# Performance work log

Hardware: AMD Instinct MI355X
Metric: run time of the kernel (lower is better)

Reference implementation:

```python
import jax, jax.numpy as jnp
import numpy as np

B, C_IN, N, F_OUT = 16, 128, 2048, 64
NEG_SLOPE = 0.33
MASK_VAL = -9e15


def setup_inputs() -> dict:
    key = jax.random.key(0)
    k1, k2, k3, k4 = jax.random.split(key, 4)
    h = jax.random.normal(k1, (B, C_IN, N, 1), dtype=jnp.float32)
    g = jax.random.normal(k2, (B, 1, N, N), dtype=jnp.float32)
    # xavier_uniform with gain=1.414
    gain = 1.414
    lim_W = gain * np.sqrt(6.0 / (C_IN + F_OUT))
    W = jax.random.uniform(k3, (C_IN, F_OUT), minval=-lim_W, maxval=lim_W, dtype=jnp.float32)
    lim_a = gain * np.sqrt(6.0 / (2 * F_OUT + 1))
    a = jax.random.uniform(k4, (2 * F_OUT, 1), minval=-lim_a, maxval=lim_a, dtype=jnp.float32)
    return {"h": h, "g": g, "W": W, "a": a}


def reference(h, g, W, a):
    # h: [B, C, N, 1] -> node features [B, N, C]
    hn = jnp.transpose(h[..., 0], (0, 2, 1))
    Wh = jnp.einsum('bnc,cf->bnf', hn, W)  # [B, N, F]
    F = W.shape[1]
    a1, a2 = a[:F, 0], a[F:, 0]
    # additive attention: e[i,j] = leakyrelu(Wh[i]@a1 + Wh[j]@a2)
    e = jax.nn.leaky_relu((Wh @ a1)[:, :, None] + (Wh @ a2)[:, None, :], NEG_SLOPE)  # [B,N,N]
    mask = g[:, 0] > 0  # [B, N, N]
    attn = jax.nn.softmax(jnp.where(mask, e, MASK_VAL), axis=-1)
    h_prime = jnp.einsum('bij,bjf->bif', attn, Wh)  # [B, N, F]
    return jnp.transpose(h_prime, (0, 2, 1))[..., None]  # [B, F, N, 1]
```

## Files before the change

### kernel.cpp

```cpp
#include <hip/hip_runtime.h>
#include <hip/hip_bf16.h>

#define NB 16
#define NC 128
#define NN 2048
#define NF 64
#define NEG_SLOPE 0.33f
#define EXP_K 1.4426950408889634f

typedef float    f32x2 __attribute__((ext_vector_type(2)));
typedef float    f32x4 __attribute__((ext_vector_type(4)));
typedef _Float16 f16x4 __attribute__((ext_vector_type(4)));
typedef _Float16 f16x8 __attribute__((ext_vector_type(8)));

__device__ __forceinline__ float lrelu(float x) {
    return fmaxf(x, x * NEG_SLOPE);
}
__device__ __forceinline__ float rdfl(float v) {
    return __int_as_float(__builtin_amdgcn_readfirstlane(__float_as_int(v)));
}

__global__ __launch_bounds__(256) void k_precompute(
    const float* __restrict__ h, const float* __restrict__ W,
    const float* __restrict__ a, _Float16* __restrict__ wht,
    float* __restrict__ s1g, float* __restrict__ s2g)
{
    __shared__ float Wl[64 * 64];
    __shared__ float ht[64 * 129];

    const int t = threadIdx.x;
    const int b = blockIdx.x >> 5;
    const int n0 = (blockIdx.x & 31) << 6;
    const int lane = t & 63, cg = t >> 6;

    #pragma unroll 8
    for (int k = 0; k < 32; ++k) {
        const int c = cg * 32 + k;
        ht[lane * 129 + c] = h[(size_t)(b * NC + c) * NN + n0 + lane];
    }

    const int fg = t & 15, ns = t >> 4;
    f32x4 acc[4] = {};
    for (int half = 0; half < 2; ++half) {
        if (half) __syncthreads();
        #pragma unroll
        for (int k = 0; k < 4; ++k) {
            const int idx = k * 1024 + t * 4;
            *(f32x4*)&Wl[idx] = *(const f32x4*)&W[half * 4096 + idx];
        }
        __syncthreads();
        #pragma unroll 4
        for (int c2 = 0; c2 < 64; ++c2) {
            const f32x4 wv = *(const f32x4*)&Wl[c2 * 64 + fg * 4];
            #pragma unroll
            for (int m = 0; m < 4; ++m) {
                const float hv = ht[(ns * 4 + m) * 129 + half * 64 + c2];
                acc[m] += wv * hv;
            }
        }
    }

    const f32x4 a1v = *(const f32x4*)&a[fg * 4];
    const f32x4 a2v = *(const f32x4*)&a[NF + fg * 4];
    #pragma unroll
    for (int m = 0; m < 4; ++m) {
        float p1 = acc[m].x * a1v.x + acc[m].y * a1v.y + acc[m].z * a1v.z + acc[m].w * a1v.w;
        float p2 = acc[m].x * a2v.x + acc[m].y * a2v.y + acc[m].z * a2v.z + acc[m].w * a2v.w;
        #pragma unroll
        for (int d = 1; d < 16; d <<= 1) {
            p1 += __shfl_xor(p1, d, 64);
            p2 += __shfl_xor(p2, d, 64);
        }
        if (fg == 0) {
            const int n = n0 + ns * 4 + m;
            s1g[(size_t)b * NN + n] = p1;
            s2g[(size_t)b * NN + n] = p2;
        }
    }
    #pragma unroll
    for (int q = 0; q < 4; ++q) {
        f16x4 v;
        v[0] = (_Float16)acc[0][q]; v[1] = (_Float16)acc[1][q];
        v[2] = (_Float16)acc[2][q]; v[3] = (_Float16)acc[3][q];
        const int f = fg * 4 + q;
        *(f16x4*)&wht[((size_t)b * NF + f) * NN + n0 + ns * 4] = v;
    }
}

__global__ __launch_bounds__(256, 4) void k_attn(
    const float* __restrict__ g, const _Float16* __restrict__ wht,
    const float* __restrict__ s1g, const float* __restrict__ s2g,
    float* __restrict__ out)
{
    __shared__ float s2b[NN];
    __shared__ float s1b[64];
    __shared__ float wred[4];
    __shared__ __align__(16) _Float16 Pc[4][1024];

    const int t = threadIdx.x;
    const int lane = t & 63;
    const int w = t >> 6;

    const int p = blockIdx.x;
    const int b = (p & 7) + ((p >> 8) << 3);
    const int strip = (p >> 3) & 31;
    const int i0 = strip * 64 + w * 16;

    f32x4 sA = *(const f32x4*)&s2g[(size_t)b * NN + t * 8];
    f32x4 sB = *(const f32x4*)&s2g[(size_t)b * NN + t * 8 + 4];
    sA *= EXP_K; sB *= EXP_K;
    *(f32x4*)&s2b[t * 8] = sA;
    *(f32x4*)&s2b[t * 8 + 4] = sB;
    if (t < 64) s1b[t] = s1g[(size_t)b * NN + strip * 64 + t] * EXP_K;
    float lm = fmaxf(fmaxf(fmaxf(sA.x, sA.y), fmaxf(sA.z, sA.w)),
                     fmaxf(fmaxf(sB.x, sB.y), fmaxf(sB.z, sB.w)));
    #pragma unroll
    for (int d = 1; d < 64; d <<= 1) lm = fmaxf(lm, __shfl_xor(lm, d, 64));
    if (lane == 0) wred[w] = lm;
    __syncthreads();
    const float S2MAX = fmaxf(fmaxf(wred[0], wred[1]), fmaxf(wred[2], wred[3]));

    float s1r[16], M[16];
    #pragma unroll
    for (int r = 0; r < 16; ++r) {
        const float v = s1b[w * 16 + r];
        s1r[r] = rdfl(v);
        M[r]   = rdfl(lrelu(v + S2MAX));
    }

    const float* gp = g + (size_t)b * NN * NN + (size_t)i0 * NN + lane;
    const int fc = lane & 15, kg = lane >> 4;
    const _Float16* wb = wht + ((size_t)b * NF + fc) * NN + kg * 8;
    char* pcb = (char*)&Pc[w][0];

    f32x4 acc0 = {0,0,0,0}, acc1 = {0,0,0,0}, acc2 = {0,0,0,0}, acc3 = {0,0,0,0};
    f32x4 acc_s = {0,0,0,0};
    f16x8 ones;
    #pragma unroll
    for (int u = 0; u < 8; ++u) ones[u] = (_Float16)1.0f;

    float ga[16], gb[16];
    #pragma unroll
    for (int r = 0; r < 16; ++r) ga[r] = gp[(size_t)r * NN];

#define CHUNK_BODY(CH, CUR, NXT)                                               \
    {                                                                          \
                                           \
        f16x8 bfv[2][4];                                                       \
        _Pragma("unroll")                                                      \
        for (int ks = 0; ks < 2; ++ks) {                                       \
            _Pragma("unroll")                                                  \
            for (int ft = 0; ft < 4; ++ft)                                     \
                bfv[ks][ft] = *(const f16x8*)(wb + (size_t)ft * 16 * NN        \
                                              + (CH) * 64 + ks * 32);          \
        }                                                                      \
        __builtin_amdgcn_sched_barrier(0);                                     \
                                            \
        if ((CH) < 31) {                                                       \
            _Pragma("unroll")                                                  \
            for (int r = 0; r < 16; ++r)                                       \
                NXT[r] = gp[(size_t)r * NN + ((CH) + 1) * 64];                 \
        }                                                                      \
        __builtin_amdgcn_sched_barrier(0);                                     \
               \
        const float sv = s2b[(CH) * 64 + lane];                                \
        _Pragma("unroll")                                                      \
        for (int r = 0; r < 16; ++r) {                                         \
            const float arg = lrelu(s1r[r] + sv) - M[r];                       \
            const float pe  = (CUR[r] > 0.0f) ? __builtin_amdgcn_exp2f(arg) : 0.0f; \
            *(_Float16*)(pcb + ((r * 128 + lane * 2) ^ ((r & 7) << 4))) = (_Float16)pe; \
        }                                                                      \
                            \
        _Pragma("unroll")                                                      \
        for (int ks = 0; ks < 2; ++ks) {                                       \
            const f16x8 af = *(const f16x8*)(pcb +                             \
                ((fc * 128 + ks * 64 + kg * 16) ^ ((fc & 7) << 4)));           \
            acc0  = __builtin_amdgcn_mfma_f32_16x16x32_f16(af, bfv[ks][0], acc0, 0, 0, 0); \
            acc1  = __builtin_amdgcn_mfma_f32_16x16x32_f16(af, bfv[ks][1], acc1, 0, 0, 0); \
            acc2  = __builtin_amdgcn_mfma_f32_16x16x32_f16(af, bfv[ks][2], acc2, 0, 0, 0); \
            acc3  = __builtin_amdgcn_mfma_f32_16x16x32_f16(af, bfv[ks][3], acc3, 0, 0, 0); \
            acc_s = __builtin_amdgcn_mfma_f32_16x16x32_f16(af, ones,       acc_s, 0, 0, 0); \
        }                                                                      \
    }

    #pragma unroll 1
    for (int it = 0; it < 16; ++it) {
        CHUNK_BODY(it * 2,     ga, gb);
        CHUNK_BODY(it * 2 + 1, gb, ga);
    }
#undef CHUNK_BODY

    f32x4 rinv;
    #pragma unroll
    for (int q = 0; q < 4; ++q) rinv[q] = 1.0f / acc_s[q];

    const size_t ob = ((size_t)b * NF + fc) * NN + (size_t)i0 + kg * 4;
    f32x4 o0, o1, o2, o3;
    #pragma unroll
    for (int q = 0; q < 4; ++q) {
        o0[q] = acc0[q] * rinv[q];
        o1[q] = acc1[q] * rinv[q];
        o2[q] = acc2[q] * rinv[q];
        o3[q] = acc3[q] * rinv[q];
    }
    *(f32x4*)&out[ob]                   = o0;
    *(f32x4*)&out[ob + (size_t)16 * NN] = o1;
    *(f32x4*)&out[ob + (size_t)32 * NN] = o2;
    *(f32x4*)&out[ob + (size_t)48 * NN] = o3;
}

extern "C" void kernel_launch(void* const* d_in, const int* in_sizes, int n_in,
                              void* d_out, int out_size, void* d_ws, size_t ws_size,
                              hipStream_t stream)
{
    (void)in_sizes; (void)n_in; (void)out_size; (void)ws_size;
    const float* h = (const float*)d_in[0];
    const float* g = (const float*)d_in[1];
    const float* W = (const float*)d_in[2];
    const float* a = (const float*)d_in[3];
    float* out = (float*)d_out;

    char* ws = (char*)d_ws;
    _Float16* wht = (_Float16*)ws;
    float* s1 = (float*)(ws + (size_t)NB * NF * NN * sizeof(_Float16));
    float* s2 = s1 + (size_t)NB * NN;

    k_precompute<<<NB * (NN / 64), 256, 0, stream>>>(h, W, a, wht, s1, s2);
    k_attn<<<NB * (NN / 64), 256, 0, stream>>>(g, wht, s1, s2, out);
}
```

Before: 94.02 us.

## Split attention key range across wave pairs and reduce partial accumulators in LDS

Each block now covers 32 query rows instead of 64. The four waves form two row groups times two halves of the key dimension, each wave handling 1024 columns, and the partial MFMA accumulators are summed through shared memory before normalisation. The grid doubles to 1024 blocks to raise parallelism. The g reads become two-float vector loads with a prefetch distance of two chunks. The cost is an extra LDS reduction and barrier, and the s2 and wht loads per block are amortised over fewer rows.

Measured after the change: 175.2 us. 1.86x slower.

```diff
diff --git a/kernel.cpp b/kernel.cpp
--- a/kernel.cpp
+++ b/kernel.cpp
@@ -10,14 +10,12 @@
 
 typedef float    f32x2 __attribute__((ext_vector_type(2)));
 typedef float    f32x4 __attribute__((ext_vector_type(4)));
+typedef _Float16 f16x2 __attribute__((ext_vector_type(2)));
 typedef _Float16 f16x4 __attribute__((ext_vector_type(4)));
 typedef _Float16 f16x8 __attribute__((ext_vector_type(8)));
 
 __device__ __forceinline__ float lrelu(float x) {
     return fmaxf(x, x * NEG_SLOPE);
-}
-__device__ __forceinline__ float rdfl(float v) {
-    return __int_as_float(__builtin_amdgcn_readfirstlane(__float_as_int(v)));
 }
 
 __global__ __launch_bounds__(256) void k_precompute(
@@ -93,25 +91,27 @@
     float* __restrict__ out)
 {
     __shared__ float s2b[NN];
-    __shared__ float s1b[64];
+    __shared__ float s1b[32];
     __shared__ float wred[4];
     __shared__ __align__(16) _Float16 Pc[4][1024];
+    __shared__ f32x4 accS[2][5][64];
 
     const int t = threadIdx.x;
     const int lane = t & 63;
     const int w = t >> 6;
+    const int rg = w & 1, jq = w >> 1;
 
     const int p = blockIdx.x;
-    const int b = (p & 7) + ((p >> 8) << 3);
-    const int strip = (p >> 3) & 31;
-    const int i0 = strip * 64 + w * 16;
+    const int b = (p & 7) + ((p >> 9) << 3);
+    const int strip = (p >> 3) & 63;
+    const int i0 = strip * 32 + rg * 16;
 
     f32x4 sA = *(const f32x4*)&s2g[(size_t)b * NN + t * 8];
     f32x4 sB = *(const f32x4*)&s2g[(size_t)b * NN + t * 8 + 4];
     sA *= EXP_K; sB *= EXP_K;
     *(f32x4*)&s2b[t * 8] = sA;
     *(f32x4*)&s2b[t * 8 + 4] = sB;
-    if (t < 64) s1b[t] = s1g[(size_t)b * NN + strip * 64 + t] * EXP_K;
+    if (t < 32) s1b[t] = s1g[(size_t)b * NN + strip * 32 + t] * EXP_K;
     float lm = fmaxf(fmaxf(fmaxf(sA.x, sA.y), fmaxf(sA.z, sA.w)),
                      fmaxf(fmaxf(sB.x, sB.y), fmaxf(sB.z, sB.w)));
     #pragma unroll
@@ -120,17 +120,19 @@
     __syncthreads();
     const float S2MAX = fmaxf(fmaxf(wred[0], wred[1]), fmaxf(wred[2], wred[3]));
 
-    float s1r[16], M[16];
-    #pragma unroll
-    for (int r = 0; r < 16; ++r) {
-        const float v = s1b[w * 16 + r];
-        s1r[r] = rdfl(v);
-        M[r]   = rdfl(lrelu(v + S2MAX));
-    }
-
-    const float* gp = g + (size_t)b * NN * NN + (size_t)i0 * NN + lane;
+    const int rh = lane >> 5;
+    const int cp = lane & 31;
+    float s1u[8], Mu[8];
+    #pragma unroll
+    for (int u = 0; u < 8; ++u) {
+        const float v = s1b[rg * 16 + u * 2 + rh];
+        s1u[u] = v;
+        Mu[u]  = lrelu(v + S2MAX);
+    }
+
+    const float* gp = g + (size_t)b * NN * NN + (size_t)i0 * NN + jq * 1024 + cp * 2;
     const int fc = lane & 15, kg = lane >> 4;
-    const _Float16* wb = wht + ((size_t)b * NF + fc) * NN + kg * 8;
+    const _Float16* wb = wht + ((size_t)b * NF + fc) * NN + jq * 1024 + kg * 8;
     char* pcb = (char*)&Pc[w][0];
 
     f32x4 acc0 = {0,0,0,0}, acc1 = {0,0,0,0}, acc2 = {0,0,0,0}, acc3 = {0,0,0,0};
@@ -139,13 +141,15 @@
     #pragma unroll
     for (int u = 0; u < 8; ++u) ones[u] = (_Float16)1.0f;
 
-    float ga[16], gb[16];
-    #pragma unroll
-    for (int r = 0; r < 16; ++r) ga[r] = gp[(size_t)r * NN];
-
-#define CHUNK_BODY(CH, CUR, NXT)                                               \
+    f32x2 gA[8], gB[8];
+    #pragma unroll
+    for (int u = 0; u < 8; ++u) gA[u] = *(const f32x2*)(gp + (size_t)(u * 2 + rh) * NN);
+    #pragma unroll
+    for (int u = 0; u < 8; ++u) gB[u] = *(const f32x2*)(gp + (size_t)(u * 2 + rh) * NN + 64);
+
+#define CHUNK_BODY(CH, CUR)                                                    \
     {                                                                          \
-                                           \
+         \
         f16x8 bfv[2][4];                                                       \
         _Pragma("unroll")                                                      \
         for (int ks = 0; ks < 2; ++ks) {                                       \
@@ -155,21 +159,27 @@
                                               + (CH) * 64 + ks * 32);          \
         }                                                                      \
         __builtin_amdgcn_sched_barrier(0);                                     \
-                                            \
-        if ((CH) < 31) {                                                       \
+                   \
+        const f32x2 sv = *(const f32x2*)&s2b[jq * 1024 + (CH) * 64 + cp * 2];  \
+        _Pragma("unroll")                                                      \
+        for (int u = 0; u < 8; ++u) {                                          \
+            const int row = u * 2 + rh;                                        \
+            const float p0 = (CUR[u].x > 0.0f)                                 \
+                ? __builtin_amdgcn_exp2f(lrelu(s1u[u] + sv.x) - Mu[u]) : 0.0f; \
+            const float p1 = (CUR[u].y > 0.0f)                                 \
+                ? __builtin_amdgcn_exp2f(lrelu(s1u[u] + sv.y) - Mu[u]) : 0.0f; \
+            f16x2 pv; pv[0] = (_Float16)p0; pv[1] = (_Float16)p1;              \
+            *(f16x2*)(pcb + ((row * 128 + cp * 4) ^ ((row & 7) << 4))) = pv;   \
+        }                                                                      \
+        __builtin_amdgcn_sched_barrier(0);                                     \
+              \
+        if ((CH) < 14) {                                                       \
             _Pragma("unroll")                                                  \
-            for (int r = 0; r < 16; ++r)                                       \
-                NXT[r] = gp[(size_t)r * NN + ((CH) + 1) * 64];                 \
+            for (int u = 0; u < 8; ++u)                                        \
+                CUR[u] = *(const f32x2*)(gp + (size_t)(u * 2 + rh) * NN        \
+                                         + ((CH) + 2) * 64);                   \
         }                                                                      \
         __builtin_amdgcn_sched_barrier(0);                                     \
-               \
-        const float sv = s2b[(CH) * 64 + lane];                                \
-        _Pragma("unroll")                                                      \
-        for (int r = 0; r < 16; ++r) {                                         \
-            const float arg = lrelu(s1r[r] + sv) - M[r];                       \
-            const float pe  = (CUR[r] > 0.0f) ? __builtin_amdgcn_exp2f(arg) : 0.0f; \
-            *(_Float16*)(pcb + ((r * 128 + lane * 2) ^ ((r & 7) << 4))) = (_Float16)pe; \
-        }                                                                      \
                             \
         _Pragma("unroll")                                                      \
         for (int ks = 0; ks < 2; ++ks) {                                       \
@@ -184,29 +194,44 @@
     }
 
     #pragma unroll 1
-    for (int it = 0; it < 16; ++it) {
-        CHUNK_BODY(it * 2,     ga, gb);
-        CHUNK_BODY(it * 2 + 1, gb, ga);
+    for (int it = 0; it < 8; ++it) {
+        CHUNK_BODY(it * 2,     gA);
+        CHUNK_BODY(it * 2 + 1, gB);
     }
 #undef CHUNK_BODY
 
-    f32x4 rinv;
-    #pragma unroll
-    for (int q = 0; q < 4; ++q) rinv[q] = 1.0f / acc_s[q];
-
-    const size_t ob = ((size_t)b * NF + fc) * NN + (size_t)i0 + kg * 4;
-    f32x4 o0, o1, o2, o3;
-    #pragma unroll
-    for (int q = 0; q < 4; ++q) {
-        o0[q] = acc0[q] * rinv[q];
-        o1[q] = acc1[q] * rinv[q];
-        o2[q] = acc2[q] * rinv[q];
-        o3[q] = acc3[q] * rinv[q];
-    }
-    *(f32x4*)&out[ob]                   = o0;
-    *(f32x4*)&out[ob + (size_t)16 * NN] = o1;
-    *(f32x4*)&out[ob + (size_t)32 * NN] = o2;
-    *(f32x4*)&out[ob + (size_t)48 * NN] = o3;
+    if (jq == 1) {
+        accS[rg][0][lane] = acc0;
+        accS[rg][1][lane] = acc1;
+        accS[rg][2][lane] = acc2;
+        accS[rg][3][lane] = acc3;
+        accS[rg][4][lane] = acc_s;
+    }
+    __syncthreads();
+    if (jq == 0) {
+        acc0  += accS[rg][0][lane];
+        acc1  += accS[rg][1][lane];
+        acc2  += accS[rg][2][lane];
+        acc3  += accS[rg][3][lane];
+        acc_s += accS[rg][4][lane];
+        f32x4 rinv;
+        #pragma unroll
+        for (int q = 0; q < 4; ++q) rinv[q] = 1.0f / acc_s[q];
+
+        const size_t ob = ((size_t)b * NF + fc) * NN + (size_t)i0 + kg * 4;
+        f32x4 o0, o1, o2, o3;
+        #pragma unroll
+        for (int q = 0; q < 4; ++q) {
+            o0[q] = acc0[q] * rinv[q];
+            o1[q] = acc1[q] * rinv[q];
+            o2[q] = acc2[q] * rinv[q];
+            o3[q] = acc3[q] * rinv[q];
+        }
+        *(f32x4*)&out[ob]                   = o0;
+        *(f32x4*)&out[ob + (size_t)16 * NN] = o1;
+        *(f32x4*)&out[ob + (size_t)32 * NN] = o2;
+        *(f32x4*)&out[ob + (size_t)48 * NN] = o3;
+    }
 }
 
 extern "C" void kernel_launch(void* const* d_in, const int* in_sizes, int n_in,
@@ -226,5 +251,5 @@
     float* s2 = s1 + (size_t)NB * NN;
 
     k_precompute<<<NB * (NN / 64), 256, 0, stream>>>(h, W, a, wht, s1, s2);
-    k_attn<<<NB * (NN / 64), 256, 0, stream>>>(g, wht, s1, s2, out);
-}
+    k_attn<<<NB * (NN / 32) * 2 / 2, 256, 0, stream>>>(g, wht, s1, s2, out);
+}
```
